# Kernel tuning notes

Measured on AMD Instinct MI355X. Metric: run time of the kernel, lower is better.

Reference implementation:

```python
import jax, jax.numpy as jnp
import numpy as np

EPS = 1e-5

def _ln(x, w, b, axes):
    mu = jnp.mean(x, axis=axes, keepdims=True)
    var = jnp.mean((x - mu) ** 2, axis=axes, keepdims=True)
    return (x - mu) / jnp.sqrt(var + EPS) * w + b

def setup_inputs() -> dict:
    key = jax.random.key(0)
    ks = jax.random.split(key, 6)
    B, L, D, A, H, F = 1, 1024, 512, 32, 8, 2048
    s = 0.02
    return {
        "x": jax.random.normal(ks[0], (B, L, D), jnp.float32),
        "ln0_w": jnp.ones((D,), jnp.float32),
        "ln0_b": jnp.zeros((D,), jnp.float32),
        "ln1_w": jnp.ones((D, H), jnp.float32),
        "ln1_b": jnp.zeros((D, H), jnp.float32),
        "qw": jax.random.normal(ks[1], (D, A * H), jnp.float32) * s,
        "qb": jnp.zeros((A * H,), jnp.float32),
        "kw": jax.random.normal(ks[2], (D, A * H), jnp.float32) * s,
        "kb": jnp.zeros((A * H,), jnp.float32),
        "vw": jax.random.normal(ks[3], (D, D * H), jnp.float32) * s,
        "vb": jnp.zeros((D * H,), jnp.float32),
        "w1": jax.random.normal(ks[4], (D * H, F), jnp.float32) * s,
        "b1": jnp.zeros((F,), jnp.float32),
        "w2": jax.random.normal(ks[5], (F, D), jnp.float32) * s,
        "b2": jnp.zeros((D,), jnp.float32),
    }

def reference(x, ln0_w, ln0_b, ln1_w, ln1_b, qw, qb, kw, kb, vw, vb, w1, b1, w2, b2):
    B, L, D = x.shape
    H = ln1_w.shape[-1]
    _x = _ln(x, ln0_w, ln0_b, -1)
    # q, k: [B, L, d_att, H] with exp(clamp(.)) feature map
    q = jnp.exp(jnp.clip(_x @ qw + qb, -10.0, 10.0)).reshape(B, L, -1, H)
    k = jnp.exp(jnp.clip(_x @ kw + kb, -10.0, 10.0)).reshape(B, L, -1, H)
    # v uses raw x (not layernormed): [B, L, D, H]
    v = (x @ vw + vb).reshape(B, L, D, H)
    # cumulative outer-product KV state: [B, L, d_att, D, H]
    kv = jnp.cumsum(jnp.einsum('blah,bldh->bladh', k, v), axis=1)
    qkv = jnp.einsum('blah,bladh->bldh', q, kv)          # [B, L, D, H]
    den = jnp.einsum('blah,blah->blh', q, jnp.cumsum(k, axis=1))[..., None, :]  # [B, L, 1, H]
    y = x[..., None] + _ln(qkv / den, ln1_w, ln1_b, (-2, -1))  # LN over (D, H) jointly
    y = y.reshape(B, L, D * H)
    h1 = jax.nn.relu(y @ w1 + b1)
    return jax.nn.relu(h1 @ w2 + b2) + x
```

## Files before the change

kernel.cpp:

```cpp
#include <hip/hip_runtime.h>
#include <hip/hip_bf16.h>
#include <math.h>

#define L_SEQ 1024
#define D_DIM 512
#define A_DIM 32
#define H_DIM 8
#define F_DIM 2048
#define AH 256
#define DH 4096
#define NC 16
#define CH 64
#define EPS_LN 1e-5f

typedef __attribute__((ext_vector_type(8))) short short8;
typedef __attribute__((ext_vector_type(4))) short short4v;
typedef __attribute__((ext_vector_type(4))) float floatx4;

#define ASYNC_COPY16(gp, lp)                                                     \
    __builtin_amdgcn_global_load_lds(                                            \
        (const __attribute__((address_space(1))) void*)(const void*)(gp),        \
        (__attribute__((address_space(3))) void*)(void*)(lp), 16, 0, 0)

__global__ __launch_bounds__(256) void prep_kernel(const float* __restrict__ x,
                                                   const float* __restrict__ ln0w,
                                                   const float* __restrict__ ln0b,
                                                   const float* __restrict__ ln1w,
                                                   const float* __restrict__ ln1b,
                                                   const float* __restrict__ qw,
                                                   const float* __restrict__ kw,
                                                   const float* __restrict__ vw,
                                                   const float* __restrict__ w1,
                                                   const float* __restrict__ w2,
                                                   __hip_bfloat16* __restrict__ xn,
                                                   __hip_bfloat16* __restrict__ xb,
                                                   __hip_bfloat16* __restrict__ qkwt,
                                                   __hip_bfloat16* __restrict__ vwt,
                                                   __hip_bfloat16* __restrict__ w1t,
                                                   __hip_bfloat16* __restrict__ w2t,
                                                   float* __restrict__ wp,
                                                   float* __restrict__ bp) {
    __shared__ float tt[32][33];
    __shared__ float red[8];
    int bid = blockIdx.x;
    int tid = threadIdx.x;
    if (bid < 1024) {
        int l = bid;
        float v0 = x[l * D_DIM + tid];
        float v1 = x[l * D_DIM + 256 + tid];
        float s = v0 + v1, s2 = v0 * v0 + v1 * v1;
        for (int off = 32; off > 0; off >>= 1) {
            s += __shfl_down(s, off);
            s2 += __shfl_down(s2, off);
        }
        int lane = tid & 63, wid = tid >> 6;
        if (lane == 0) { red[wid] = s; red[4 + wid] = s2; }
        __syncthreads();
        float ts = red[0] + red[1] + red[2] + red[3];
        float t2 = red[4] + red[5] + red[6] + red[7];
        float mu = ts / (float)D_DIM;
        float var = t2 / (float)D_DIM - mu * mu;
        float rs = rsqrtf(var + EPS_LN);
        xn[l * D_DIM + tid]       = (__hip_bfloat16)((v0 - mu) * rs * ln0w[tid] + ln0b[tid]);
        xn[l * D_DIM + 256 + tid] = (__hip_bfloat16)((v1 - mu) * rs * ln0w[256 + tid] + ln0b[256 + tid]);
        xb[l * D_DIM + tid]       = (__hip_bfloat16)v0;
        xb[l * D_DIM + 256 + tid] = (__hip_bfloat16)v1;
        return;
    }
    if (bid == 12544) {
        int e0 = tid * 16;
        float o1[16], o2[16];
#pragma unroll
        for (int j = 0; j < 16; ++j) {
            int ee = e0 + j;
            int pi = ((ee & 511) << 3) | (ee >> 9);
            o1[j] = ln1w[pi];
            o2[j] = ln1b[pi];
        }
#pragma unroll
        for (int j = 0; j < 4; ++j) {
            *(float4*)(wp + e0 + j * 4) = *(float4*)&o1[j * 4];
            *(float4*)(bp + e0 + j * 4) = *(float4*)&o2[j * 4];
        }
        return;
    }
    const float* in;
    __hip_bfloat16* out;
    int R, C, mode = 0, t;
    if (bid < 1152)      { t = bid - 1024;  in = qw; out = qkwt;                      R = 512;  C = 256; }
    else if (bid < 1280) { t = bid - 1152;  in = kw; out = qkwt + (size_t)AH * D_DIM; R = 512;  C = 256; }
    else if (bid < 3328) { t = bid - 1280;  in = vw; out = vwt;  mode = 1;            R = 512;  C = 4096; }
    else if (bid < 11520){ t = bid - 3328;  in = w1; out = w1t;  mode = 2;            R = 4096; C = 2048; }
    else                 { t = bid - 11520; in = w2; out = w2t;                       R = 2048; C = 512; }
    int ctiles = C >> 5;
    int cx = t % ctiles, cy = t / ctiles;
    int tx = tid & 31, ti = tid >> 5;
    int r0 = cy * 32, c0 = cx * 32;
#pragma unroll
    for (int ii = 0; ii < 4; ++ii) {
        int rr = r0 + ti + ii * 8;
        if (mode == 2) rr = ((rr & 511) << 3) | (rr >> 9);
        tt[ti + ii * 8][tx] = in[(size_t)rr * C + c0 + tx];
    }
    __syncthreads();
#pragma unroll
    for (int ii = 0; ii < 4; ++ii) {
        int c = c0 + ti + ii * 8;
        int orow = (mode == 1) ? (((c & 7) << 9) | (c >> 3)) : c;
        out[(size_t)orow * R + r0 + tx] = (__hip_bfloat16)tt[tx][ti + ii * 8];
    }
}

__device__ __forceinline__ void gemm_core(const __hip_bfloat16* __restrict__ A,
                                          const __hip_bfloat16* __restrict__ Bt,
                                          int K, int bm, int bn, int k_beg, int k_end,
                                          __hip_bfloat16* As, __hip_bfloat16* Bs,
                                          floatx4 acc[2][2]) {
    const int tid = threadIdx.x;
    const int w = tid >> 6, lane = tid & 63;
    const int wm = (w >> 1) * 32, wn = (w & 1) * 32;
    const int quad = lane >> 4, l16 = lane & 15;
    const int srow = tid >> 4, sslot = tid & 15;
    const int scg = sslot ^ srow;
    for (int k0 = k_beg; k0 < k_end; k0 += 128) {
        __syncthreads();
#pragma unroll
        for (int j = 0; j < 4; ++j) {
            ASYNC_COPY16(A + (size_t)(bm + j * 16 + srow) * K + k0 + scg * 8,
                         As + j * 2048 + w * 512);
            ASYNC_COPY16(Bt + (size_t)(bn + j * 16 + srow) * K + k0 + scg * 8,
                         Bs + j * 2048 + w * 512);
        }
        __syncthreads();
#pragma unroll
        for (int ks = 0; ks < 4; ++ks) {
            short8 af[2], bfr[2];
#pragma unroll
            for (int mt = 0; mt < 2; ++mt) {
                int rr = wm + mt * 16 + l16;
                af[mt] = *(const short8*)(As + rr * 128 + (((ks * 4 + quad) ^ (rr & 15)) * 8));
            }
#pragma unroll
            for (int nt = 0; nt < 2; ++nt) {
                int rr = wn + nt * 16 + l16;
                bfr[nt] = *(const short8*)(Bs + rr * 128 + (((ks * 4 + quad) ^ (rr & 15)) * 8));
            }
#pragma unroll
            for (int mt = 0; mt < 2; ++mt)
#pragma unroll
                for (int nt = 0; nt < 2; ++nt)
                    acc[mt][nt] = __builtin_amdgcn_mfma_f32_16x16x32_bf16(
                        af[mt], bfr[nt], acc[mt][nt], 0, 0, 0);
        }
    }
}

__global__ __launch_bounds__(256) void qkv_gemm(const __hip_bfloat16* __restrict__ xn,
                                                const __hip_bfloat16* __restrict__ xb,
                                                const __hip_bfloat16* __restrict__ qkwt,
                                                const __hip_bfloat16* __restrict__ vwt,
                                                const float* __restrict__ qb,
                                                const float* __restrict__ kb,
                                                const float* __restrict__ vb,
                                                __hip_bfloat16* __restrict__ q2,
                                                __hip_bfloat16* __restrict__ k2,
                                                __hip_bfloat16* __restrict__ vT) {
    __shared__ __align__(16) __hip_bfloat16 As[64 * 128];
    __shared__ __align__(16) __hip_bfloat16 Bs[64 * 128];
    const int tid = threadIdx.x;
    const int w = tid >> 6, lane = tid & 63;
    const int wm = (w >> 1) * 32, wn = (w & 1) * 32;
    const int quad = lane >> 4, l16 = lane & 15;
    int bid = blockIdx.x;
    bool isv = bid < 1024;
    const __hip_bfloat16 *A, *Bt;
    int bx, by;
    if (isv) {
        int r = bid >> 3;
        bx = (bid & 7) * 8 + (r & 7);
        by = r >> 3;
        A = xb; Bt = vwt;
    } else {
        int b2 = bid - 1024;
        bx = b2 & 7; by = b2 >> 3;
        A = xn; Bt = qkwt;
    }
    const int bm = by * 64, bn = bx * 64;
    floatx4 acc[2][2];
#pragma unroll
    for (int i = 0; i < 2; ++i)
#pragma unroll
        for (int j = 0; j < 2; ++j) acc[i][j] = (floatx4)0.f;
    gemm_core(A, Bt, D_DIM, bm, bn, 0, D_DIM, As, Bs, acc);
    if (isv) {
        __syncthreads();
        __hip_bfloat16* Ct = As;
#pragma unroll
        for (int mt = 0; mt < 2; ++mt)
#pragma unroll
            for (int nt = 0; nt < 2; ++nt) {
                int col = bn + wn + nt * 16 + l16;
                int bi = ((col & 511) << 3) | (col >> 9);
                float bbv = vb[bi];
                __hip_bfloat16 tmp[4];
#pragma unroll
                for (int r = 0; r < 4; ++r)
                    tmp[r] = (__hip_bfloat16)(acc[mt][nt][r] + bbv);
                *(short4v*)&Ct[(wn + nt * 16 + l16) * 72 + wm + mt * 16 + quad * 4] =
                    *(short4v*)tmp;
            }
        __syncthreads();
        int colloc = tid >> 2, seg = (tid & 3) * 16;
        short8 o0 = *(const short8*)&Ct[colloc * 72 + seg];
        short8 o1 = *(const short8*)&Ct[colloc * 72 + seg + 8];
        *(short8*)(vT + (size_t)(bn + colloc) * 1024 + bm + seg) = o0;
        *(short8*)(vT + (size_t)(bn + colloc) * 1024 + bm + seg + 8) = o1;
    } else {
        __syncthreads();
        __hip_bfloat16* q2t = As;
        bool isq = bn < 256;
        const float* bias = isq ? qb : kb;
        int cb = isq ? bn : bn - 256;
#pragma unroll
        for (int mt = 0; mt < 2; ++mt)
#pragma unroll
            for (int nt = 0; nt < 2; ++nt) {
                int colloc = wn + nt * 16 + l16;
                float bb = bias[cb + colloc];
                int hh = colloc & 7, aa = colloc >> 3;
#pragma unroll
                for (int r = 0; r < 4; ++r) {
                    int rowloc = wm + mt * 16 + quad * 4 + r;
                    float val = expf(fminf(fmaxf(acc[mt][nt][r] + bb, -10.f), 10.f));
                    q2t[((hh * 64 + rowloc) << 3) + aa] = (__hip_bfloat16)val;
                }
            }
        __syncthreads();
        __hip_bfloat16* dst = isq ? q2 : k2;
        int a0 = cb >> 3;
#pragma unroll
        for (int j = 0; j < 2; ++j) {
            int p = tid + j * 256;
            int hh = p >> 6, ll = p & 63;
            short8 o = *(const short8*)&q2t[(hh * 64 + ll) << 3];
            *(short8*)(dst + (size_t)(hh * 1024 + bm + ll) * 32 + a0) = o;
        }
    }
}

template <int STRIP>
__global__ __launch_bounds__(256) void gemm_split(const __hip_bfloat16* __restrict__ A,
                                                  const __hip_bfloat16* __restrict__ Bt,
                                                  float* __restrict__ part,
                                                  int M, int N, int K, int Ksub) {
    __shared__ __align__(16) __hip_bfloat16 As[64 * 128];
    __shared__ __align__(16) __hip_bfloat16 Bs[64 * 128];
    const int tid = threadIdx.x;
    const int w = tid >> 6, lane = tid & 63;
    const int wm = (w >> 1) * 32, wn = (w & 1) * 32;
    const int quad = lane >> 4, l16 = lane & 15;
    int bid = blockIdx.x;
    int r = bid >> 3;
    int bx = (bid & 7) * STRIP + (r % STRIP);
    int by = r / STRIP;
    const int bm = by * 64, bn = bx * 64;
    const int kz = blockIdx.z;
    floatx4 acc[2][2];
#pragma unroll
    for (int i = 0; i < 2; ++i)
#pragma unroll
        for (int j = 0; j < 2; ++j) acc[i][j] = (floatx4)0.f;
    gemm_core(A, Bt, K, bm, bn, kz * Ksub, kz * Ksub + Ksub, As, Bs, acc);
#pragma unroll
    for (int mt = 0; mt < 2; ++mt)
#pragma unroll
        for (int nt = 0; nt < 2; ++nt)
#pragma unroll
            for (int rr = 0; rr < 4; ++rr) {
                int row = bm + wm + mt * 16 + quad * 4 + rr;
                int col = bn + wn + nt * 16 + l16;
                part[((size_t)kz * M + row) * N + col] = acc[mt][nt][rr];
            }
}

__global__ __launch_bounds__(256) void w1red(const float* __restrict__ part,
                                             const float* __restrict__ b1,
                                             __hip_bfloat16* __restrict__ h1) {
    size_t e = ((size_t)blockIdx.x * 256 + threadIdx.x) * 4;
    const size_t MN = (size_t)L_SEQ * F_DIM;
    float4 p0 = *(const float4*)(part + e);
    float4 p1 = *(const float4*)(part + MN + e);
    float4 bb = *(const float4*)(b1 + (e & (F_DIM - 1)));
    h1[e + 0] = (__hip_bfloat16)fmaxf(p0.x + p1.x + bb.x, 0.f);
    h1[e + 1] = (__hip_bfloat16)fmaxf(p0.y + p1.y + bb.y, 0.f);
    h1[e + 2] = (__hip_bfloat16)fmaxf(p0.z + p1.z + bb.z, 0.f);
    h1[e + 3] = (__hip_bfloat16)fmaxf(p0.w + p1.w + bb.w, 0.f);
}

__global__ __launch_bounds__(256) void w2red(const float* __restrict__ part,
                                             const float* __restrict__ b2,
                                             const float* __restrict__ x,
                                             float* __restrict__ out) {
    size_t e = ((size_t)blockIdx.x * 256 + threadIdx.x) * 4;
    const size_t MN = (size_t)L_SEQ * D_DIM;
    float4 v0 = *(const float4*)(part + e);
    float4 v1 = *(const float4*)(part + MN + e);
    float4 v2 = *(const float4*)(part + 2 * MN + e);
    float4 v3 = *(const float4*)(part + 3 * MN + e);
    float4 bb = *(const float4*)(b2 + (e & 511));
    float4 xx = *(const float4*)(x + e);
    float4 r;
    r.x = fmaxf(v0.x + v1.x + v2.x + v3.x + bb.x, 0.f) + xx.x;
    r.y = fmaxf(v0.y + v1.y + v2.y + v3.y + bb.y, 0.f) + xx.y;
    r.z = fmaxf(v0.z + v1.z + v2.z + v3.z + bb.z, 0.f) + xx.z;
    r.w = fmaxf(v0.w + v1.w + v2.w + v3.w + bb.w, 0.f) + xx.w;
    *(float4*)(out + e) = r;
}

__global__ __launch_bounds__(256) void kvchunk_kernel(const __hip_bfloat16* __restrict__ k2,
                                                      const __hip_bfloat16* __restrict__ vT,
                                                      float* __restrict__ S,
                                                      float* __restrict__ Ka) {
    int c = blockIdx.x, h = blockIdx.y, dq = blockIdx.z;
    int tid = threadIdx.x;
    __shared__ __align__(16) __hip_bfloat16 kaT[32][72];
    __shared__ __align__(16) float St[128][36];
    {
        int l = tid >> 2, a0s = (tid & 3) * 8;
        short8 kv8 = *(const short8*)(k2 + (size_t)(h * 1024 + c * 64 + l) * 32 + a0s);
#pragma unroll
        for (int j = 0; j < 8; ++j)
            kaT[a0s + j][l] = ((const __hip_bfloat16*)&kv8)[j];
    }
    __syncthreads();
    int w = tid >> 6, lane = tid & 63, quad = lane >> 4, l16 = lane & 15;
    floatx4 acc[2][2];
#pragma unroll
    for (int i = 0; i < 2; ++i)
#pragma unroll
        for (int j = 0; j < 2; ++j) acc[i][j] = (floatx4)0.f;
#pragma unroll
    for (int ks = 0; ks < 2; ++ks) {
        short8 af[2], bfr[2];
#pragma unroll
        for (int mt = 0; mt < 2; ++mt)
            af[mt] = *(const short8*)&kaT[mt * 16 + l16][ks * 32 + quad * 8];
#pragma unroll
        for (int nt = 0; nt < 2; ++nt)
            bfr[nt] = *(const short8*)(vT + (size_t)(h * 512 + dq * 128 + w * 32 + nt * 16 + l16) * 1024
                                       + c * 64 + ks * 32 + quad * 8);
#pragma unroll
        for (int mt = 0; mt < 2; ++mt)
#pragma unroll
            for (int nt = 0; nt < 2; ++nt)
                acc[mt][nt] = __builtin_amdgcn_mfma_f32_16x16x32_bf16(
                    af[mt], bfr[nt], acc[mt][nt], 0, 0, 0);
    }
#pragma unroll
    for (int mt = 0; mt < 2; ++mt)
#pragma unroll
        for (int nt = 0; nt < 2; ++nt)
            *(floatx4*)&St[w * 32 + nt * 16 + l16][mt * 16 + quad * 4] = acc[mt][nt];
    __syncthreads();
    int d = tid >> 1, aseg = (tid & 1) * 16;
    float* dst = S + (size_t)((c * 8 + h) * 512 + dq * 128 + d) * 32 + aseg;
    const float* src = &St[d][aseg];
#pragma unroll
    for (int j = 0; j < 4; ++j)
        *(float4*)(dst + j * 4) = *(const float4*)(src + j * 4);
    if (dq == 0 && tid < 32) {
        float s = 0.f;
        for (int l = 0; l < CH; ++l) s += (float)kaT[tid][l];
        Ka[c * AH + tid * 8 + h] = s;
    }
}

__global__ __launch_bounds__(256) void scan_kernel(const float* __restrict__ S,
                                                   const float* __restrict__ Ka,
                                                   __hip_bfloat16* __restrict__ P2,
                                                   float* __restrict__ KaP) {
    size_t j = ((size_t)blockIdx.x * 256 + threadIdx.x) * 4;
    const size_t CS = 8 * 512 * 32;
    float4 run = {0.f, 0.f, 0.f, 0.f};
    for (int c = 0; c < NC; ++c) {
        __hip_bfloat16 o[4] = {(__hip_bfloat16)run.x, (__hip_bfloat16)run.y,
                               (__hip_bfloat16)run.z, (__hip_bfloat16)run.w};
        *(short4v*)&P2[c * CS + j] = *(short4v*)o;
        float4 sv = *(const float4*)(S + c * CS + j);
        run.x += sv.x; run.y += sv.y; run.z += sv.z; run.w += sv.w;
    }
    if (blockIdx.x == 0) {
        int t = threadIdx.x;
        float rk = 0.f;
        for (int c = 0; c < NC; ++c) {
            KaP[c * AH + t] = rk;
            rk += Ka[c * AH + t];
        }
    }
}

__global__ __launch_bounds__(256) void passC_kernel(const __hip_bfloat16* __restrict__ q2,
                                                    const __hip_bfloat16* __restrict__ k2,
                                                    const __hip_bfloat16* __restrict__ vT,
                                                    const __hip_bfloat16* __restrict__ P2,
                                                    const float* __restrict__ KaP,
                                                    __hip_bfloat16* __restrict__ qkv,
                                                    float* __restrict__ den) {
    int c = blockIdx.x, h = blockIdx.y, dq = blockIdx.z;
    int tid = threadIdx.x;
    __shared__ __align__(16) __hip_bfloat16 Sc[64][72];
    __shared__ float KaPs[32];
    if (dq == 0 && tid < 32) KaPs[tid] = KaP[c * AH + tid * 8 + h];
    int w = tid >> 6, lane = tid & 63, quad = lane >> 4, l16 = lane & 15;
    const size_t qbase = (size_t)(h * 1024 + c * 64) * 32;
    short8 afq = *(const short8*)(q2 + qbase + (w * 16 + l16) * 32 + quad * 8);
    floatx4 sacc[4];
#pragma unroll
    for (int nt = 0; nt < 4; ++nt) sacc[nt] = (floatx4)0.f;
#pragma unroll
    for (int nt = 0; nt < 4; ++nt) {
        short8 bfr = *(const short8*)(k2 + qbase + (nt * 16 + l16) * 32 + quad * 8);
        sacc[nt] = __builtin_amdgcn_mfma_f32_16x16x32_bf16(afq, bfr, sacc[nt], 0, 0, 0);
    }
#pragma unroll
    for (int nt = 0; nt < 4; ++nt)
#pragma unroll
        for (int r = 0; r < 4; ++r) {
            int l = w * 16 + quad * 4 + r;
            int lp = nt * 16 + l16;
            Sc[l][lp] = (__hip_bfloat16)((lp <= l) ? sacc[nt][r] : 0.f);
        }
    __syncthreads();
    if (dq == 0 && tid < 64) {
        int l = tid;
        float s = 0.f;
        for (int lp = 0; lp <= l; ++lp) s += (float)Sc[l][lp];
        const __hip_bfloat16* qp = q2 + qbase + l * 32;
        for (int a = 0; a < A_DIM; ++a) s += (float)qp[a] * KaPs[a];
        den[(c * CH + l) * H_DIM + h] = s;
    }
    floatx4 acc[8];
#pragma unroll
    for (int nt = 0; nt < 8; ++nt) acc[nt] = (floatx4)0.f;
#pragma unroll
    for (int nt = 0; nt < 8; ++nt) {
        short8 pb = *(const short8*)(P2 + ((size_t)((c * 8 + h) * 512 + dq * 128 + nt * 16 + l16)) * 32 + quad * 8);
        acc[nt] = __builtin_amdgcn_mfma_f32_16x16x32_bf16(afq, pb, acc[nt], 0, 0, 0);
    }
#pragma unroll
    for (int ks = 0; ks < 2; ++ks) {
        short8 afs = *(const short8*)&Sc[w * 16 + l16][ks * 32 + quad * 8];
#pragma unroll
        for (int nt = 0; nt < 8; ++nt) {
            short8 bfr = *(const short8*)(vT + (size_t)(h * 512 + dq * 128 + nt * 16 + l16) * 1024
                                          + c * 64 + ks * 32 + quad * 8);
            acc[nt] = __builtin_amdgcn_mfma_f32_16x16x32_bf16(afs, bfr, acc[nt], 0, 0, 0);
        }
    }
#pragma unroll
    for (int nt = 0; nt < 8; ++nt)
#pragma unroll
        for (int r = 0; r < 4; ++r) {
            int l = w * 16 + quad * 4 + r;
            int d = dq * 128 + nt * 16 + l16;
            qkv[(size_t)(c * CH + l) * DH + h * D_DIM + d] = (__hip_bfloat16)acc[nt][r];
        }
}

__global__ __launch_bounds__(256) void ln1_kernel(const __hip_bfloat16* __restrict__ qkv,
                                                  const float* __restrict__ den,
                                                  const float* __restrict__ x,
                                                  const float* __restrict__ wp,
                                                  const float* __restrict__ bp,
                                                  __hip_bfloat16* __restrict__ y) {
    int l = blockIdx.x, tid = threadIdx.x;
    __shared__ float red[8];
    int h = tid >> 5;
    int e0 = tid * 16;
    int d0 = e0 & 511;
    float rden = 1.f / den[l * 8 + h];
    short8 v0 = *(const short8*)(qkv + (size_t)l * DH + e0);
    short8 v1 = *(const short8*)(qkv + (size_t)l * DH + e0 + 8);
    float vals[16];
    float s = 0.f, s2 = 0.f;
#pragma unroll
    for (int j = 0; j < 8; ++j) {
        vals[j] = (float)((const __hip_bfloat16*)&v0)[j] * rden;
        vals[8 + j] = (float)((const __hip_bfloat16*)&v1)[j] * rden;
    }
#pragma unroll
    for (int j = 0; j < 16; ++j) { s += vals[j]; s2 += vals[j] * vals[j]; }
    for (int off = 32; off > 0; off >>= 1) {
        s += __shfl_down(s, off);
        s2 += __shfl_down(s2, off);
    }
    int lane = tid & 63, wid = tid >> 6;
    if (lane == 0) { red[wid] = s; red[4 + wid] = s2; }
    __syncthreads();
    float ts = red[0] + red[1] + red[2] + red[3];
    float t2 = red[4] + red[5] + red[6] + red[7];
    float mu = ts / (float)DH;
    float var = t2 / (float)DH - mu * mu;
    float rs = rsqrtf(var + EPS_LN);
    __hip_bfloat16 o[16];
#pragma unroll
    for (int j4 = 0; j4 < 4; ++j4) {
        float4 xx = *(const float4*)(x + l * D_DIM + d0 + j4 * 4);
        float4 wv = *(const float4*)(wp + e0 + j4 * 4);
        float4 bv = *(const float4*)(bp + e0 + j4 * 4);
        o[j4 * 4 + 0] = (__hip_bfloat16)(xx.x + (vals[j4 * 4 + 0] - mu) * rs * wv.x + bv.x);
        o[j4 * 4 + 1] = (__hip_bfloat16)(xx.y + (vals[j4 * 4 + 1] - mu) * rs * wv.y + bv.y);
        o[j4 * 4 + 2] = (__hip_bfloat16)(xx.z + (vals[j4 * 4 + 2] - mu) * rs * wv.z + bv.z);
        o[j4 * 4 + 3] = (__hip_bfloat16)(xx.w + (vals[j4 * 4 + 3] - mu) * rs * wv.w + bv.w);
    }
    *(short8*)(y + (size_t)l * DH + e0) = *(short8*)&o[0];
    *(short8*)(y + (size_t)l * DH + e0 + 8) = *(short8*)&o[8];
}

extern "C" void kernel_launch(void* const* d_in, const int* in_sizes, int n_in,
                              void* d_out, int out_size, void* d_ws, size_t ws_size,
                              hipStream_t stream) {
    const float* x     = (const float*)d_in[0];
    const float* ln0_w = (const float*)d_in[1];
    const float* ln0_b = (const float*)d_in[2];
    const float* ln1_w = (const float*)d_in[3];
    const float* ln1_b = (const float*)d_in[4];
    const float* qw    = (const float*)d_in[5];
    const float* qb    = (const float*)d_in[6];
    const float* kw    = (const float*)d_in[7];
    const float* kb    = (const float*)d_in[8];
    const float* vw    = (const float*)d_in[9];
    const float* vb    = (const float*)d_in[10];
    const float* w1    = (const float*)d_in[11];
    const float* b1    = (const float*)d_in[12];
    const float* w2    = (const float*)d_in[13];
    const float* b2    = (const float*)d_in[14];
    float* out = (float*)d_out;

    char* ws = (char*)d_ws;
    __hip_bfloat16* xn_bf = (__hip_bfloat16*)(ws + 0);
    __hip_bfloat16* xbf   = (__hip_bfloat16*)(ws + 1048576);
    __hip_bfloat16* qkwt  = (__hip_bfloat16*)(ws + 2097152);
    __hip_bfloat16* vwt   = (__hip_bfloat16*)(ws + 2621440);
    __hip_bfloat16* w1t   = (__hip_bfloat16*)(ws + 6815744);
    __hip_bfloat16* w2t   = (__hip_bfloat16*)(ws + 23592960);
    __hip_bfloat16* q2    = (__hip_bfloat16*)(ws + 25690112);
    __hip_bfloat16* k2    = (__hip_bfloat16*)(ws + 26214400);
    __hip_bfloat16* vT    = (__hip_bfloat16*)(ws + 26738688);
    float* S              = (float*)(ws + 35127296);
    __hip_bfloat16* P2    = (__hip_bfloat16*)(ws + 43515904);
    __hip_bfloat16* qkvb  = (__hip_bfloat16*)(ws + 51904512);
    float* Ka  = (float*)(ws + 60293120);
    float* KaP = (float*)(ws + 60309504);
    float* den = (float*)(ws + 60325888);
    float* wp  = (float*)(ws + 60358656);
    float* bp  = (float*)(ws + 60375040);
    float* w1part = (float*)(ws + 60391424);
    __hip_bfloat16* y  = P2;
    __hip_bfloat16* h1 = (__hip_bfloat16*)S;
    float* w2part = (float*)qkvb;

    prep_kernel<<<12545, 256, 0, stream>>>(x, ln0_w, ln0_b, ln1_w, ln1_b,
                                           qw, kw, vw, w1, w2,
                                           xn_bf, xbf, qkwt, vwt, w1t, w2t, wp, bp);
    qkv_gemm<<<1152, 256, 0, stream>>>(xn_bf, xbf, qkwt, vwt, qb, kb, vb, q2, k2, vT);
    kvchunk_kernel<<<dim3(NC, H_DIM, 4), 256, 0, stream>>>(k2, vT, S, Ka);
    scan_kernel<<<128, 256, 0, stream>>>(S, Ka, P2, KaP);
    passC_kernel<<<dim3(NC, H_DIM, 4), 256, 0, stream>>>(q2, k2, vT, P2, KaP, qkvb, den);
    ln1_kernel<<<L_SEQ, 256, 0, stream>>>(qkvb, den, x, wp, bp, y);
    gemm_split<4><<<dim3(512, 1, 2), 256, 0, stream>>>(y, w1t, w1part,
                                                       L_SEQ, F_DIM, DH, DH / 2);
    w1red<<<(L_SEQ * F_DIM) / 1024, 256, 0, stream>>>(w1part, b1, h1);
    gemm_split<1><<<dim3(128, 1, 4), 256, 0, stream>>>(h1, w2t, w2part,
                                                       L_SEQ, D_DIM, F_DIM, F_DIM / 4);
    w2red<<<(L_SEQ * D_DIM) / 1024, 256, 0, stream>>>(w2part, b2, x, out);

    (void)in_sizes; (void)n_in; (void)out_size; (void)ws_size;
}
```

Baseline: 206.2 us.

## Replace split-K W1 GEMM and reduction with single-pass 64x32-tile GEMM

Templates the shared GEMM core on the N tile width and adds a w1_gemm kernel that uses 64x32 tiles across the full K=4096. Bias and ReLU are fused into its epilogue, writing bf16 h1 directly. This drops the split-K fp32 partial buffer and the separate w1red pass, saving 16 MB of writes plus the reads back. In exchange, each block runs a serial K loop twice as long with narrower B tiles, so there is less reuse per A load and each wave issues fewer MFMAs per LDS fetch.

```diff
diff --git a/kernel.cpp b/kernel.cpp
--- a/kernel.cpp
+++ b/kernel.cpp
@@ -111,44 +111,47 @@
     }
 }
 
+template <int BN>
 __device__ __forceinline__ void gemm_core(const __hip_bfloat16* __restrict__ A,
                                           const __hip_bfloat16* __restrict__ Bt,
                                           int K, int bm, int bn, int k_beg, int k_end,
                                           __hip_bfloat16* As, __hip_bfloat16* Bs,
-                                          floatx4 acc[2][2]) {
+                                          floatx4 (&acc)[2][BN / 32]) {
+    constexpr int NT = BN / 32;
     const int tid = threadIdx.x;
     const int w = tid >> 6, lane = tid & 63;
-    const int wm = (w >> 1) * 32, wn = (w & 1) * 32;
+    const int wm = (w >> 1) * 32, wn = (w & 1) * (BN / 2);
     const int quad = lane >> 4, l16 = lane & 15;
     const int srow = tid >> 4, sslot = tid & 15;
     const int scg = sslot ^ srow;
     for (int k0 = k_beg; k0 < k_end; k0 += 128) {
         __syncthreads();
 #pragma unroll
-        for (int j = 0; j < 4; ++j) {
+        for (int j = 0; j < 4; ++j)
             ASYNC_COPY16(A + (size_t)(bm + j * 16 + srow) * K + k0 + scg * 8,
                          As + j * 2048 + w * 512);
+#pragma unroll
+        for (int j = 0; j < BN / 16; ++j)
             ASYNC_COPY16(Bt + (size_t)(bn + j * 16 + srow) * K + k0 + scg * 8,
                          Bs + j * 2048 + w * 512);
-        }
         __syncthreads();
 #pragma unroll
         for (int ks = 0; ks < 4; ++ks) {
-            short8 af[2], bfr[2];
+            short8 af[2], bfr[NT];
 #pragma unroll
             for (int mt = 0; mt < 2; ++mt) {
                 int rr = wm + mt * 16 + l16;
                 af[mt] = *(const short8*)(As + rr * 128 + (((ks * 4 + quad) ^ (rr & 15)) * 8));
             }
 #pragma unroll
-            for (int nt = 0; nt < 2; ++nt) {
+            for (int nt = 0; nt < NT; ++nt) {
                 int rr = wn + nt * 16 + l16;
                 bfr[nt] = *(const short8*)(Bs + rr * 128 + (((ks * 4 + quad) ^ (rr & 15)) * 8));
             }
 #pragma unroll
             for (int mt = 0; mt < 2; ++mt)
 #pragma unroll
-                for (int nt = 0; nt < 2; ++nt)
+                for (int nt = 0; nt < NT; ++nt)
                     acc[mt][nt] = __builtin_amdgcn_mfma_f32_16x16x32_bf16(
                         af[mt], bfr[nt], acc[mt][nt], 0, 0, 0);
         }
@@ -191,7 +194,7 @@
     for (int i = 0; i < 2; ++i)
 #pragma unroll
         for (int j = 0; j < 2; ++j) acc[i][j] = (floatx4)0.f;
-    gemm_core(A, Bt, D_DIM, bm, bn, 0, D_DIM, As, Bs, acc);
+    gemm_core<64>(A, Bt, D_DIM, bm, bn, 0, D_DIM, As, Bs, acc);
     if (isv) {
         __syncthreads();
         __hip_bfloat16* Ct = As;
@@ -246,6 +249,37 @@
             *(short8*)(dst + (size_t)(hh * 1024 + bm + ll) * 32 + a0) = o;
         }
     }
+}
+
+__global__ __launch_bounds__(256) void w1_gemm(const __hip_bfloat16* __restrict__ y,
+                                               const __hip_bfloat16* __restrict__ w1t,
+                                               const float* __restrict__ b1,
+                                               __hip_bfloat16* __restrict__ h1) {
+    __shared__ __align__(16) __hip_bfloat16 As[64 * 128];
+    __shared__ __align__(16) __hip_bfloat16 Bs[32 * 128];
+    const int tid = threadIdx.x;
+    const int w = tid >> 6, lane = tid & 63;
+    const int wm = (w >> 1) * 32, wn = (w & 1) * 16;
+    const int quad = lane >> 4, l16 = lane & 15;
+    int bid = blockIdx.x;
+    int r = bid >> 3;
+    int bx = (bid & 7) * 8 + (r & 7);
+    int by = r >> 3;
+    const int bm = by * 64, bn = bx * 32;
+    floatx4 acc[2][1];
+    acc[0][0] = (floatx4)0.f;
+    acc[1][0] = (floatx4)0.f;
+    gemm_core<32>(y, w1t, DH, bm, bn, 0, DH, As, Bs, acc);
+    int col = bn + wn + l16;
+    float bb = b1[col];
+#pragma unroll
+    for (int mt = 0; mt < 2; ++mt)
+#pragma unroll
+        for (int rr = 0; rr < 4; ++rr) {
+            int row = bm + wm + mt * 16 + quad * 4 + rr;
+            h1[(size_t)row * F_DIM + col] =
+                (__hip_bfloat16)fmaxf(acc[mt][0][rr] + bb, 0.f);
+        }
 }
 
 template <int STRIP>
@@ -270,7 +304,7 @@
     for (int i = 0; i < 2; ++i)
 #pragma unroll
         for (int j = 0; j < 2; ++j) acc[i][j] = (floatx4)0.f;
-    gemm_core(A, Bt, K, bm, bn, kz * Ksub, kz * Ksub + Ksub, As, Bs, acc);
+    gemm_core<64>(A, Bt, K, bm, bn, kz * Ksub, kz * Ksub + Ksub, As, Bs, acc);
 #pragma unroll
     for (int mt = 0; mt < 2; ++mt)
 #pragma unroll
@@ -281,20 +315,6 @@
                 int col = bn + wn + nt * 16 + l16;
                 part[((size_t)kz * M + row) * N + col] = acc[mt][nt][rr];
             }
-}
-
-__global__ __launch_bounds__(256) void w1red(const float* __restrict__ part,
-                                             const float* __restrict__ b1,
-                                             __hip_bfloat16* __restrict__ h1) {
-    size_t e = ((size_t)blockIdx.x * 256 + threadIdx.x) * 4;
-    const size_t MN = (size_t)L_SEQ * F_DIM;
-    float4 p0 = *(const float4*)(part + e);
-    float4 p1 = *(const float4*)(part + MN + e);
-    float4 bb = *(const float4*)(b1 + (e & (F_DIM - 1)));
-    h1[e + 0] = (__hip_bfloat16)fmaxf(p0.x + p1.x + bb.x, 0.f);
-    h1[e + 1] = (__hip_bfloat16)fmaxf(p0.y + p1.y + bb.y, 0.f);
-    h1[e + 2] = (__hip_bfloat16)fmaxf(p0.z + p1.z + bb.z, 0.f);
-    h1[e + 3] = (__hip_bfloat16)fmaxf(p0.w + p1.w + bb.w, 0.f);
 }
 
 __global__ __launch_bounds__(256) void w2red(const float* __restrict__ part,
@@ -555,7 +575,6 @@
     float* den = (float*)(ws + 60325888);
     float* wp  = (float*)(ws + 60358656);
     float* bp  = (float*)(ws + 60375040);
-    float* w1part = (float*)(ws + 60391424);
     __hip_bfloat16* y  = P2;
     __hip_bfloat16* h1 = (__hip_bfloat16*)S;
     float* w2part = (float*)qkvb;
@@ -568,9 +587,7 @@
     scan_kernel<<<128, 256, 0, stream>>>(S, Ka, P2, KaP);
     passC_kernel<<<dim3(NC, H_DIM, 4), 256, 0, stream>>>(q2, k2, vT, P2, KaP, qkvb, den);
     ln1_kernel<<<L_SEQ, 256, 0, stream>>>(qkvb, den, x, wp, bp, y);
-    gemm_split<4><<<dim3(512, 1, 2), 256, 0, stream>>>(y, w1t, w1part,
-                                                       L_SEQ, F_DIM, DH, DH / 2);
-    w1red<<<(L_SEQ * F_DIM) / 1024, 256, 0, stream>>>(w1part, b1, h1);
+    w1_gemm<<<1024, 256, 0, stream>>>(y, w1t, b1, h1);
     gemm_split<1><<<dim3(128, 1, 4), 256, 0, stream>>>(h1, w2t, w2part,
                                                        L_SEQ, D_DIM, F_DIM, F_DIM / 4);
     w2red<<<(L_SEQ * D_DIM) / 1024, 256, 0, stream>>>(w2part, b2, x, out);
```

Result: no change. 204.6 us (-0.7%).
